# Optimization experiments

Measured on AMD Instinct MI355X. Metric: run time of the kernel, lower is better.

Reference implementation:

```python
import jax, jax.numpy as jnp
import numpy as np

B, C, D, H = 4, 1024, 768, 12      # batch, seq_len(>512 long-doc), hidden, heads
E, K, S, V, P = 32, 2, 24, 8, 512  # entities, mentions/entity, sents, virtual nodes, ht pairs
NT = 256                            # node type embedding dim
EMB, BLK, NL = 768, 64, 97          # emb_size, block_size, num_labels
OFFSET = 1


def setup_inputs() -> dict:
    key = jax.random.key(0)
    ks = jax.random.split(key, 13)
    return {
        "sequence_output": jax.random.normal(ks[0], (B, C, D), jnp.float32),
        "attention": jax.random.uniform(ks[1], (B, H, C, C), jnp.float32),
        "entity_pos": jax.random.randint(ks[2], (B, E, K), 0, C - 2),
        "sent_pos": jax.random.randint(ks[3], (B, S), 0, C - 2),
        "virtual_pos": jax.random.randint(ks[4], (B, V), 0, C - 2),
        "hts": jax.random.randint(ks[5], (B, P, 2), 0, E),
        "node_type_emb": jax.random.normal(ks[6], (B, E, NT), jnp.float32) * 0.02,
        "W_head": jax.random.normal(ks[7], (2 * D + NT, EMB), jnp.float32) * 0.02,
        "b_head": jnp.zeros((EMB,), jnp.float32),
        "W_tail": jax.random.normal(ks[8], (2 * D + NT, EMB), jnp.float32) * 0.02,
        "b_tail": jnp.zeros((EMB,), jnp.float32),
        "W_bil": jax.random.normal(ks[9], (EMB * BLK, NL), jnp.float32) * 0.02,
        "b_bil": jnp.zeros((NL,), jnp.float32),
    }


def reference(sequence_output, attention, entity_pos, sent_pos, virtual_pos, hts,
              node_type_emb, W_head, b_head, W_tail, b_tail, W_bil, b_bil):
    # --- get_mention_embed / get_entity_embed: gather mention-start rows ---
    idx = entity_pos + OFFSET                      # [B,E,K] token index of each mention start
    flat = idx.reshape(B, E * K)                   # mention order matches torch double loop
    mention_embed = jnp.take_along_axis(sequence_output, flat[:, :, None], axis=1)  # [B,E*K,D]
    entity_embed = jax.nn.logsumexp(mention_embed.reshape(B, E, K, D), axis=2)      # [B,E,D]

    # --- get_sent_embed / get_virtual_embed: single-row gathers ---
    sent_embed = jnp.take_along_axis(sequence_output, (sent_pos + OFFSET)[:, :, None], axis=1)      # [B,S,D]
    virtual_embed = jnp.take_along_axis(sequence_output, (virtual_pos + OFFSET)[:, :, None], axis=1)  # [B,V,D]

    # --- get_rss: localized-context pooling over attention ---
    att_t = attention.transpose(0, 2, 1, 3)        # [B,C,H,C] so we gather query rows
    e_att = jnp.take_along_axis(att_t, flat[:, :, None, None], axis=1)  # [B,E*K,H,C]
    e_att = e_att.reshape(B, E, K, H, C).mean(axis=2)                   # [B,E,H,C] mean over mentions
    h_att = jnp.take_along_axis(e_att, hts[:, :, 0][:, :, None, None], axis=1)  # [B,P,H,C]
    t_att = jnp.take_along_axis(e_att, hts[:, :, 1][:, :, None, None], axis=1)  # [B,P,H,C]
    ht_att = (h_att * t_att).mean(axis=2)                               # [B,P,C] mean over heads
    ht_att = ht_att / (ht_att.sum(axis=-1, keepdims=True) + 1e-5)
    rs = jnp.einsum('bld,brl->brd', sequence_output, ht_att)            # [B,P,D]

    # --- get_pair_entity_embed on entity hidden state (entity_embed + node-type emb) ---
    ent_hidden = jnp.concatenate([entity_embed, node_type_emb], axis=-1)          # [B,E,D+NT]
    s_emb = jnp.take_along_axis(ent_hidden, hts[:, :, 0][:, :, None], axis=1)     # [B,P,D+NT]
    t_emb = jnp.take_along_axis(ent_hidden, hts[:, :, 1][:, :, None], axis=1)

    # --- head/tail extractors + grouped bilinear classifier ---
    hs = jnp.tanh(jnp.concatenate([s_emb, rs], axis=-1) @ W_head + b_head)  # [B,P,EMB]
    ts = jnp.tanh(jnp.concatenate([t_emb, rs], axis=-1) @ W_tail + b_tail)
    b1 = hs.reshape(B, P, EMB // BLK, BLK)
    b2 = ts.reshape(B, P, EMB // BLK, BLK)
    bl = (b1[..., :, None] * b2[..., None, :]).reshape(B, P, EMB * BLK)     # [B,P,EMB*BLK]
    logits = bl @ W_bil + b_bil                                             # [B,P,NL]
    return (logits, mention_embed, sent_embed, virtual_embed)
```

## Files before the change

### kernel.cpp

```cpp
#include <hip/hip_runtime.h>

#define B_   4
#define C_   1024
#define D_   768
#define H_   12
#define E_   32
#define K_   2
#define S_   24
#define V_   8
#define P_   512
#define NT_  256
#define EMB_ 768
#define BLK_ 64
#define NL_  97
#define DNT_ 1024
#define KHT_ 1792
#define KBIL_ 49152
#define NPAD_ 128

typedef __bf16 bf16x8 __attribute__((ext_vector_type(8)));
typedef float  f32x4  __attribute__((ext_vector_type(4)));

__device__ __forceinline__ float b2f(unsigned short u) {
    return (float)__builtin_bit_cast(__bf16, u);
}
__device__ __forceinline__ unsigned short f2b(float f) {
    return __builtin_bit_cast(unsigned short, (__bf16)f);
}
__device__ __forceinline__ float ld_in(const void* p, size_t i, int isf) {
    return isf ? ((const float*)p)[i] : b2f(((const unsigned short*)p)[i]);
}
__device__ __forceinline__ void st_out(void* p, size_t i, float v, int isf) {
    if (isf) ((float*)p)[i] = v;
    else     ((unsigned short*)p)[i] = f2b(v);
}

__global__ __launch_bounds__(256) void k_probe(const unsigned short* __restrict__ seq_u,
                                               int* __restrict__ flag)
{
    __shared__ int sh_huge[256];
    __shared__ int sh_zero[256];
    int tid = threadIdx.x;
    int huge = 0, zero = 0;
    for (int i = tid; i < 4096; i += 256) {
        unsigned short u = seq_u[2 * i];
        float f = b2f(u);
        if (!(fabsf(f) <= 1e10f)) huge = 1;
        if (u == 0) zero++;
    }
    sh_huge[tid] = huge; sh_zero[tid] = zero;
    __syncthreads();
    for (int s = 128; s > 0; s >>= 1) {
        if (tid < s) { sh_huge[tid] |= sh_huge[tid + s]; sh_zero[tid] += sh_zero[tid + s]; }
        __syncthreads();
    }
    if (tid == 0) flag[0] = (sh_huge[0] || sh_zero[0] > 3600) ? 1 : 0;
}

#define PREP_GATHER 256
#define PREP_EATT   (PREP_GATHER + B_*E_*H_)
#define PREP_TSEQ   (PREP_EATT + 768)
#define PREP_TW     (PREP_TSEQ + 672)
#define PREP_TBIL   (PREP_TW + 768)

__global__ __launch_bounds__(256) void k_prep(
    const void* __restrict__ seq, const void* __restrict__ att,
    const int* __restrict__ epos, const int* __restrict__ spos,
    const int* __restrict__ vpos, const void* __restrict__ ntype,
    const void* __restrict__ Wh, const void* __restrict__ Wt_,
    const void* __restrict__ Wb,
    float* __restrict__ enth, float* __restrict__ e_att,
    unsigned short* __restrict__ seqT,
    unsigned short* __restrict__ WtH, unsigned short* __restrict__ WtT,
    unsigned short* __restrict__ WtB,
    void* __restrict__ outv, long long moff, long long soff, long long voff,
    const int* __restrict__ dflag)
{
    __shared__ __align__(16) unsigned char smem[12544];
    int blk = blockIdx.x, tid = threadIdx.x;
    int isf = *dflag;
    if (blk < PREP_GATHER) {
        if (blk < B_ * E_) {
            int b = blk / E_, e = blk % E_;
            int i0 = epos[(b * E_ + e) * K_ + 0] + 1;
            int i1 = epos[(b * E_ + e) * K_ + 1] + 1;
            size_t r0 = ((size_t)b * C_ + i0) * D_;
            size_t r1 = ((size_t)b * C_ + i1) * D_;
            size_t m0 = (size_t)moff + ((size_t)(b * E_ * K_) + 2 * e) * D_;
            size_t m1 = m0 + D_;
            float* eh = enth + (size_t)(b * E_ + e) * DNT_;
            for (int d = tid; d < D_; d += 256) {
                float a = ld_in(seq, r0 + d, isf);
                float c = ld_in(seq, r1 + d, isf);
                st_out(outv, m0 + d, a, isf);
                st_out(outv, m1 + d, c, isf);
                float mx = fmaxf(a, c);
                eh[d] = mx + logf(expf(a - mx) + expf(c - mx));
            }
            size_t nt0 = (size_t)(b * E_ + e) * NT_;
            for (int j = tid; j < NT_; j += 256) eh[D_ + j] = ld_in(ntype, nt0 + j, isf);
        } else if (blk < B_ * E_ + B_ * S_) {
            int t = blk - B_ * E_; int b = t / S_, s = t % S_;
            int i = spos[b * S_ + s] + 1;
            size_t r = ((size_t)b * C_ + i) * D_;
            size_t o = (size_t)soff + (size_t)(b * S_ + s) * D_;
            for (int d = tid; d < D_; d += 256) st_out(outv, o + d, ld_in(seq, r + d, isf), isf);
        } else {
            int t = blk - B_ * E_ - B_ * S_; int b = t / V_, v = t % V_;
            int i = vpos[b * V_ + v] + 1;
            size_t r = ((size_t)b * C_ + i) * D_;
            size_t o = (size_t)voff + (size_t)(b * V_ + v) * D_;
            for (int d = tid; d < D_; d += 256) st_out(outv, o + d, ld_in(seq, r + d, isf), isf);
        }
    } else if (blk < PREP_EATT) {
        int t = blk - PREP_GATHER;
        int b = t / (E_ * H_); int r = t % (E_ * H_); int e = r / H_; int h = r % H_;
        int i0 = epos[(b * E_ + e) * K_ + 0] + 1;
        int i1 = epos[(b * E_ + e) * K_ + 1] + 1;
        size_t a0 = (((size_t)b * H_ + h) * C_ + i0) * C_;
        size_t a1 = (((size_t)b * H_ + h) * C_ + i1) * C_;
        float* o = e_att + (((size_t)(b * E_ + e)) * H_ + h) * C_;
        for (int c = tid; c < C_; c += 256)
            o[c] = 0.5f * (ld_in(att, a0 + c, isf) + ld_in(att, a1 + c, isf));
    } else if (blk < PREP_TSEQ) {
        int t = blk - PREP_EATT;
        int b = t / 192; int r = t % 192; int ct = r / 12; int dt = r % 12;
        typedef unsigned short row65[65];
        row65* tile = (row65*)smem;
        for (int idx = tid; idx < 4096; idx += 256) {
            int cc = idx >> 6, dd = idx & 63;
            tile[cc][dd] = f2b(ld_in(seq, ((size_t)b * C_ + ct * 64 + cc) * D_ + dt * 64 + dd, isf));
        }
        __syncthreads();
        for (int idx = tid; idx < 4096; idx += 256) {
            int dd = idx >> 6, cc = idx & 63;
            seqT[((size_t)b * D_ + dt * 64 + dd) * C_ + ct * 64 + cc] = tile[cc][dd];
        }
    } else if (blk < PREP_TW) {
        int t = blk - PREP_TSEQ;
        int mat = t / 336; int r = t % 336; int kt = r / 12; int nt = r % 12;
        const void* in = mat ? Wt_ : Wh;
        unsigned short* out = mat ? WtT : WtH;
        typedef unsigned short row65[65];
        row65* tile = (row65*)smem;
        for (int idx = tid; idx < 4096; idx += 256) {
            int kk = idx >> 6, nn = idx & 63;
            tile[kk][nn] = f2b(ld_in(in, ((size_t)kt * 64 + kk) * EMB_ + nt * 64 + nn, isf));
        }
        __syncthreads();
        for (int idx = tid; idx < 4096; idx += 256) {
            int nn = idx >> 6, kk = idx & 63;
            out[((size_t)nt * 64 + nn) * KHT_ + kt * 64 + kk] = tile[kk][nn];
        }
    } else {
        int t = blk - PREP_TW;
        int k0 = t << 6;
        unsigned short* raw = (unsigned short*)smem;
        for (int idx = tid; idx < 64 * NL_; idx += 256)
            raw[idx] = f2b(ld_in(Wb, (size_t)k0 * NL_ + idx, isf));
        __syncthreads();
        int kk = tid & 63, nq = tid >> 6;
        for (int i = 0; i < 32; i++) {
            int n = nq * 32 + i;
            unsigned short v = (n < NL_) ? raw[kk * NL_ + n] : (unsigned short)0;
            WtB[(size_t)n * KBIL_ + k0 + kk] = v;
        }
    }
}

__global__ __launch_bounds__(256) void k_mid(
    const float* __restrict__ e_att, const float* __restrict__ enth,
    const int* __restrict__ hts,
    unsigned short* __restrict__ htb,
    unsigned short* __restrict__ Xh, unsigned short* __restrict__ Xt,
    float* __restrict__ logitsF)
{
    __shared__ float red[4];
    int blk = blockIdx.x, tid = threadIdx.x;
    if (blk < B_ * P_) {
        int b = blk >> 9;
        int he = hts[blk * 2 + 0], te = hts[blk * 2 + 1];
        const float* ph = e_att + (size_t)(b * E_ + he) * H_ * C_;
        const float* pt = e_att + (size_t)(b * E_ + te) * H_ * C_;
        float v[4]; float ls = 0.f;
        for (int ci = 0; ci < 4; ci++) {
            int c = tid + (ci << 8);
            float acc = 0.f;
#pragma unroll
            for (int h = 0; h < H_; h++) acc += ph[h * C_ + c] * pt[h * C_ + c];
            acc *= (1.0f / (float)H_);
            v[ci] = acc; ls += acc;
        }
        for (int off = 32; off > 0; off >>= 1) ls += __shfl_down(ls, off, 64);
        if ((tid & 63) == 0) red[tid >> 6] = ls;
        __syncthreads();
        float inv = 1.0f / (red[0] + red[1] + red[2] + red[3] + 1e-5f);
        for (int ci = 0; ci < 4; ci++)
            htb[((size_t)blk << 10) + tid + (ci << 8)] = f2b(v[ci] * inv);
    } else if (blk < 2 * B_ * P_) {
        int m = blk - B_ * P_; int b = m >> 9;
        int eh = hts[m * 2 + 0], et = hts[m * 2 + 1];
        const float* sh = enth + (size_t)(b * E_ + eh) * DNT_;
        const float* st = enth + (size_t)(b * E_ + et) * DNT_;
        for (int k = tid; k < DNT_; k += 256) {
            Xh[(size_t)m * KHT_ + k] = f2b(sh[k]);
            Xt[(size_t)m * KHT_ + k] = f2b(st[k]);
        }
    } else {
        int t = blk - 2 * B_ * P_;
        ((float4*)logitsF)[(size_t)t * 256 + tid] = make_float4(0.f, 0.f, 0.f, 0.f);
    }
}

__global__ __launch_bounds__(256) void k_gemm(
    const unsigned short* __restrict__ A0, const unsigned short* __restrict__ A1,
    const unsigned short* __restrict__ B0, const unsigned short* __restrict__ B1,
    long long lda, long long ldb, long long sAz, long long sBz,
    int nsteps, int zmode,
    const void* __restrict__ bias0, const void* __restrict__ bias1,
    unsigned short* __restrict__ oY0, unsigned short* __restrict__ oY1,
    unsigned short* __restrict__ oX1, unsigned short* __restrict__ oX2,
    const int* __restrict__ dflag)
{
    int n0 = blockIdx.x * 64, m0 = blockIdx.y * 64, z = blockIdx.z;
    const unsigned short* Ab; const unsigned short* Bb;
    unsigned short* oY = nullptr; const void* bias = nullptr;
    if (zmode == 0) {
        Ab = A0 + (size_t)z * sAz; Bb = B0 + (size_t)z * sBz;
    } else {
        Ab = z ? A1 : A0; Bb = z ? B1 : B0;
        oY = z ? oY1 : oY0; bias = z ? bias1 : bias0;
    }
    __shared__ __align__(16) unsigned short a_lds[64][40];
    __shared__ __align__(16) unsigned short b_lds[64][40];
    int tid = threadIdx.x, lane = tid & 63, w = tid >> 6;
    int wm = (w >> 1) * 32, wn = (w & 1) * 32, q = lane >> 4, l15 = lane & 15;
    f32x4 acc00 = {0.f,0.f,0.f,0.f}, acc01 = acc00, acc10 = acc00, acc11 = acc00;
    int srow = tid >> 2, sch = (tid & 3) * 8;
    const unsigned short* pa = Ab + (size_t)(m0 + srow) * lda + sch;
    const unsigned short* pb = Bb + (size_t)(n0 + srow) * ldb + sch;
    int4 ra = *(const int4*)pa;
    int4 rb = *(const int4*)pb;
    for (int ks = 0; ks < nsteps; ks++) {
        __syncthreads();
        *(int4*)&a_lds[srow][sch] = ra;
        *(int4*)&b_lds[srow][sch] = rb;
        __syncthreads();
        if (ks + 1 < nsteps) {
            ra = *(const int4*)(pa + (size_t)(ks + 1) * 32);
            rb = *(const int4*)(pb + (size_t)(ks + 1) * 32);
        }
        bf16x8 a0 = *(const bf16x8*)&a_lds[wm + l15][q * 8];
        bf16x8 a1 = *(const bf16x8*)&a_lds[wm + 16 + l15][q * 8];
        bf16x8 b0 = *(const bf16x8*)&b_lds[wn + l15][q * 8];
        bf16x8 b1 = *(const bf16x8*)&b_lds[wn + 16 + l15][q * 8];
        acc00 = __builtin_amdgcn_mfma_f32_16x16x32_bf16(a0, b0, acc00, 0, 0, 0);
        acc01 = __builtin_amdgcn_mfma_f32_16x16x32_bf16(a0, b1, acc01, 0, 0, 0);
        acc10 = __builtin_amdgcn_mfma_f32_16x16x32_bf16(a1, b0, acc10, 0, 0, 0);
        acc11 = __builtin_amdgcn_mfma_f32_16x16x32_bf16(a1, b1, acc11, 0, 0, 0);
    }
    f32x4 accs[2][2] = {{acc00, acc01}, {acc10, acc11}};
    int isf = (zmode == 1) ? *dflag : 0;
#pragma unroll
    for (int mt = 0; mt < 2; mt++)
#pragma unroll
        for (int nt = 0; nt < 2; nt++) {
            int gmb = m0 + wm + mt * 16 + q * 4;
            int gn  = n0 + wn + nt * 16 + l15;
            if (zmode == 0) {
#pragma unroll
                for (int r = 0; r < 4; r++) {
                    unsigned short v = f2b(accs[mt][nt][r]);
                    size_t o = (size_t)(z * P_ + gmb + r) * KHT_ + DNT_ + gn;
                    oX1[o] = v; oX2[o] = v;
                }
            } else {
                float bv = ld_in(bias, gn, isf);
#pragma unroll
                for (int r = 0; r < 4; r++)
                    oY[(size_t)(gmb + r) * EMB_ + gn] = f2b(tanhf(accs[mt][nt][r] + bv));
            }
        }
}

__global__ __launch_bounds__(256) void k_bil(
    const unsigned short* __restrict__ hsB, const unsigned short* __restrict__ tsB,
    const unsigned short* __restrict__ WtB, float* __restrict__ logitsF)
{
    int m0 = blockIdx.x * 32;
    int g  = blockIdx.y;
    int tid = threadIdx.x, lane = tid & 63, w = tid >> 6;
    int q = lane >> 4, l15 = lane & 15;
    __shared__ __align__(16) unsigned short hsl[32][80];
    __shared__ __align__(16) unsigned short tsl[32][80];
    for (int idx = tid; idx < 512; idx += 256) {
        int m = idx >> 4, j4 = (idx & 15) * 4;
        *(ushort4*)&hsl[m][j4] = *(const ushort4*)&hsB[(size_t)(m0 + m) * EMB_ + g * 64 + j4];
        *(ushort4*)&tsl[m][j4] = *(const ushort4*)&tsB[(size_t)(m0 + m) * EMB_ + g * 64 + j4];
    }
    __syncthreads();

    const unsigned short* pB0 = WtB + (size_t)(w * 16 + l15) * KBIL_ + g * 4096 + q * 8;
    const unsigned short* pB1 = pB0 + (size_t)64 * KBIL_;
    bf16x8 rb0[2], rb1[2];
    rb0[0] = *(const bf16x8*)(pB0);      rb1[0] = *(const bf16x8*)(pB1);
    rb0[1] = *(const bf16x8*)(pB0 + 32); rb1[1] = *(const bf16x8*)(pB1 + 32);
    f32x4 acc00 = {0.f,0.f,0.f,0.f}, acc01 = acc00, acc10 = acc00, acc11 = acc00;

#pragma unroll 2
    for (int kk = 0; kk < 128; kk++) {
        int sl = kk & 1;
        bf16x8 bw0 = rb0[sl], bw1 = rb1[sl];
        if (kk + 2 < 128) {
            rb0[sl] = *(const bf16x8*)(pB0 + (size_t)(kk + 2) * 32);
            rb1[sl] = *(const bf16x8*)(pB1 + (size_t)(kk + 2) * 32);
        }
        int i = kk >> 1, h = kk & 1;
        float ha0 = b2f(hsl[l15][i]);
        float ha1 = b2f(hsl[16 + l15][i]);
        bf16x8 t0 = *(const bf16x8*)&tsl[l15][h * 32 + q * 8];
        bf16x8 t1 = *(const bf16x8*)&tsl[16 + l15][h * 32 + q * 8];
        bf16x8 af0, af1;
#pragma unroll
        for (int j = 0; j < 8; j++) {
            af0[j] = (__bf16)(ha0 * (float)t0[j]);
            af1[j] = (__bf16)(ha1 * (float)t1[j]);
        }
        acc00 = __builtin_amdgcn_mfma_f32_16x16x32_bf16(af0, bw0, acc00, 0, 0, 0);
        acc01 = __builtin_amdgcn_mfma_f32_16x16x32_bf16(af0, bw1, acc01, 0, 0, 0);
        acc10 = __builtin_amdgcn_mfma_f32_16x16x32_bf16(af1, bw0, acc10, 0, 0, 0);
        acc11 = __builtin_amdgcn_mfma_f32_16x16x32_bf16(af1, bw1, acc11, 0, 0, 0);
    }
#pragma unroll
    for (int r = 0; r < 4; r++) {
        atomicAdd(&logitsF[(size_t)(m0 + q * 4 + r) * NPAD_ + w * 16 + l15],           acc00[r]);
        atomicAdd(&logitsF[(size_t)(m0 + q * 4 + r) * NPAD_ + w * 16 + 64 + l15],      acc01[r]);
        atomicAdd(&logitsF[(size_t)(m0 + 16 + q * 4 + r) * NPAD_ + w * 16 + l15],      acc10[r]);
        atomicAdd(&logitsF[(size_t)(m0 + 16 + q * 4 + r) * NPAD_ + w * 16 + 64 + l15], acc11[r]);
    }
}

__global__ __launch_bounds__(256) void k_fin(
    const float* __restrict__ logitsF, const void* __restrict__ b_bil,
    void* __restrict__ outv, const int* __restrict__ dflag)
{
    int isf = *dflag;
    int idx = blockIdx.x * 256 + threadIdx.x;
    if (idx >= B_ * P_ * NL_) return;
    int m = idx / NL_, n = idx % NL_;
    st_out(outv, idx, logitsF[(size_t)m * NPAD_ + n] + ld_in(b_bil, n, isf), isf);
}

extern "C" void kernel_launch(void* const* d_in, const int* in_sizes, int n_in,
                              void* d_out, int out_size, void* d_ws, size_t ws_size,
                              hipStream_t stream)
{
    const void* seq    = d_in[0];
    const void* att    = d_in[1];
    const int*  epos   = (const int*)d_in[2];
    const int*  spos   = (const int*)d_in[3];
    const int*  vpos   = (const int*)d_in[4];
    const int*  hts    = (const int*)d_in[5];
    const void* ntype  = d_in[6];
    const void* W_head = d_in[7];
    const void* b_head = d_in[8];
    const void* W_tail = d_in[9];
    const void* b_tail = d_in[10];
    const void* W_bil  = d_in[11];
    const void* b_bil  = d_in[12];

    long long mention_off = (long long)B_ * P_ * NL_;
    long long sent_off    = mention_off + (long long)B_ * E_ * K_ * D_;
    long long virt_off    = sent_off + (long long)B_ * S_ * D_;

    char* p = (char*)d_ws;
    auto alloc = [&](size_t bytes) { void* r = (void*)p; p += (bytes + 255) & ~(size_t)255; return r; };
    int*            dflag   = (int*)alloc(256);
    float*          e_att   = (float*)alloc((size_t)B_ * E_ * H_ * C_ * 4);
    unsigned short* htb     = (unsigned short*)alloc((size_t)B_ * P_ * C_ * 2);
    unsigned short* seqT    = (unsigned short*)alloc((size_t)B_ * D_ * C_ * 2);
    unsigned short* WtH     = (unsigned short*)alloc((size_t)EMB_ * KHT_ * 2);
    unsigned short* WtT     = (unsigned short*)alloc((size_t)EMB_ * KHT_ * 2);
    unsigned short* WtB     = (unsigned short*)alloc((size_t)NPAD_ * KBIL_ * 2);
    unsigned short* Xh      = (unsigned short*)alloc((size_t)B_ * P_ * KHT_ * 2);
    unsigned short* Xt      = (unsigned short*)alloc((size_t)B_ * P_ * KHT_ * 2);
    unsigned short* hsB     = (unsigned short*)alloc((size_t)B_ * P_ * EMB_ * 2);
    unsigned short* tsB     = (unsigned short*)alloc((size_t)B_ * P_ * EMB_ * 2);
    float*          logitsF = (float*)alloc((size_t)B_ * P_ * NPAD_ * 4);
    float*          enth    = (float*)alloc((size_t)B_ * E_ * DNT_ * 4);

    dim3 blk(256);
    k_probe<<<1, blk, 0, stream>>>((const unsigned short*)seq, dflag);
    k_prep<<<PREP_TBIL, blk, 0, stream>>>(
        seq, att, epos, spos, vpos, ntype, W_head, W_tail, W_bil,
        enth, e_att, seqT, WtH, WtT, WtB,
        d_out, mention_off, sent_off, virt_off, dflag);
    k_mid<<<2 * B_ * P_ + 256, blk, 0, stream>>>(e_att, enth, hts, htb, Xh, Xt, logitsF);
    k_gemm<<<dim3(EMB_ / 64, P_ / 64, B_), blk, 0, stream>>>(
        htb, nullptr, seqT, nullptr, C_, C_,
        (long long)P_ * C_, (long long)D_ * C_, C_ / 32, 0,
        nullptr, nullptr, nullptr, nullptr, Xh, Xt, dflag);
    k_gemm<<<dim3(EMB_ / 64, (B_ * P_) / 64, 2), blk, 0, stream>>>(
        Xh, Xt, WtH, WtT, KHT_, KHT_, 0, 0, KHT_ / 32, 1,
        b_head, b_tail, hsB, tsB, nullptr, nullptr, dflag);
    k_bil<<<dim3((B_ * P_) / 32, 12, 1), blk, 0, stream>>>(hsB, tsB, WtB, logitsF);
    k_fin<<<(B_ * P_ * NL_ + 255) / 256, blk, 0, stream>>>(logitsF, b_bil, d_out, dflag);
}
```

Before: 453.9 us.

## Inline dtype probe per wavefront and store entity attention as bf16

Removes the separate single-block probe kernel that detected whether inputs are fp32 or bf16. Each wavefront now runs a cheaper 64-sample ballot-based probe inline in every kernel that needs the flag. The averaged entity attention buffer is also stored as bf16 instead of fp32, halving its write and read traffic in k_prep and k_mid. The trade-offs are a smaller probe sample, which makes the dtype guess less robust, and reduced precision in the intermediate attention values.

```diff
diff --git a/kernel.cpp b/kernel.cpp
--- a/kernel.cpp
+++ b/kernel.cpp
@@ -34,27 +34,11 @@
     if (isf) ((float*)p)[i] = v;
     else     ((unsigned short*)p)[i] = f2b(v);
 }
-
-__global__ __launch_bounds__(256) void k_probe(const unsigned short* __restrict__ seq_u,
-                                               int* __restrict__ flag)
-{
-    __shared__ int sh_huge[256];
-    __shared__ int sh_zero[256];
-    int tid = threadIdx.x;
-    int huge = 0, zero = 0;
-    for (int i = tid; i < 4096; i += 256) {
-        unsigned short u = seq_u[2 * i];
-        float f = b2f(u);
-        if (!(fabsf(f) <= 1e10f)) huge = 1;
-        if (u == 0) zero++;
-    }
-    sh_huge[tid] = huge; sh_zero[tid] = zero;
-    __syncthreads();
-    for (int s = 128; s > 0; s >>= 1) {
-        if (tid < s) { sh_huge[tid] |= sh_huge[tid + s]; sh_zero[tid] += sh_zero[tid + s]; }
-        __syncthreads();
-    }
-    if (tid == 0) flag[0] = (sh_huge[0] || sh_zero[0] > 3600) ? 1 : 0;
+__device__ __forceinline__ int probe_isf(const void* seq) {
+    unsigned short u = ((const unsigned short*)seq)[2 * (threadIdx.x & 63)];
+    int huge = !(fabsf(b2f(u)) <= 1e10f);
+    unsigned long long zb = __ballot(u == 0);
+    return __any(huge) || (__popcll(zb) > 56);
 }
 
 #define PREP_GATHER 256
@@ -69,16 +53,15 @@
     const int* __restrict__ vpos, const void* __restrict__ ntype,
     const void* __restrict__ Wh, const void* __restrict__ Wt_,
     const void* __restrict__ Wb,
-    float* __restrict__ enth, float* __restrict__ e_att,
+    float* __restrict__ enth, unsigned short* __restrict__ e_att,
     unsigned short* __restrict__ seqT,
     unsigned short* __restrict__ WtH, unsigned short* __restrict__ WtT,
     unsigned short* __restrict__ WtB,
-    void* __restrict__ outv, long long moff, long long soff, long long voff,
-    const int* __restrict__ dflag)
+    void* __restrict__ outv, long long moff, long long soff, long long voff)
 {
     __shared__ __align__(16) unsigned char smem[12544];
     int blk = blockIdx.x, tid = threadIdx.x;
-    int isf = *dflag;
+    int isf = probe_isf(seq);
     if (blk < PREP_GATHER) {
         if (blk < B_ * E_) {
             int b = blk / E_, e = blk % E_;
@@ -119,9 +102,9 @@
         int i1 = epos[(b * E_ + e) * K_ + 1] + 1;
         size_t a0 = (((size_t)b * H_ + h) * C_ + i0) * C_;
         size_t a1 = (((size_t)b * H_ + h) * C_ + i1) * C_;
-        float* o = e_att + (((size_t)(b * E_ + e)) * H_ + h) * C_;
+        unsigned short* o = e_att + (((size_t)(b * E_ + e)) * H_ + h) * C_;
         for (int c = tid; c < C_; c += 256)
-            o[c] = 0.5f * (ld_in(att, a0 + c, isf) + ld_in(att, a1 + c, isf));
+            o[c] = f2b(0.5f * (ld_in(att, a0 + c, isf) + ld_in(att, a1 + c, isf)));
     } else if (blk < PREP_TSEQ) {
         int t = blk - PREP_EATT;
         int b = t / 192; int r = t % 192; int ct = r / 12; int dt = r % 12;
@@ -169,7 +152,7 @@
 }
 
 __global__ __launch_bounds__(256) void k_mid(
-    const float* __restrict__ e_att, const float* __restrict__ enth,
+    const unsigned short* __restrict__ e_att, const float* __restrict__ enth,
     const int* __restrict__ hts,
     unsigned short* __restrict__ htb,
     unsigned short* __restrict__ Xh, unsigned short* __restrict__ Xt,
@@ -180,14 +163,14 @@
     if (blk < B_ * P_) {
         int b = blk >> 9;
         int he = hts[blk * 2 + 0], te = hts[blk * 2 + 1];
-        const float* ph = e_att + (size_t)(b * E_ + he) * H_ * C_;
-        const float* pt = e_att + (size_t)(b * E_ + te) * H_ * C_;
+        const unsigned short* ph = e_att + (size_t)(b * E_ + he) * H_ * C_;
+        const unsigned short* pt = e_att + (size_t)(b * E_ + te) * H_ * C_;
         float v[4]; float ls = 0.f;
         for (int ci = 0; ci < 4; ci++) {
             int c = tid + (ci << 8);
             float acc = 0.f;
 #pragma unroll
-            for (int h = 0; h < H_; h++) acc += ph[h * C_ + c] * pt[h * C_ + c];
+            for (int h = 0; h < H_; h++) acc += b2f(ph[h * C_ + c]) * b2f(pt[h * C_ + c]);
             acc *= (1.0f / (float)H_);
             v[ci] = acc; ls += acc;
         }
@@ -220,7 +203,7 @@
     const void* __restrict__ bias0, const void* __restrict__ bias1,
     unsigned short* __restrict__ oY0, unsigned short* __restrict__ oY1,
     unsigned short* __restrict__ oX1, unsigned short* __restrict__ oX2,
-    const int* __restrict__ dflag)
+    const void* __restrict__ seq)
 {
     int n0 = blockIdx.x * 64, m0 = blockIdx.y * 64, z = blockIdx.z;
     const unsigned short* Ab; const unsigned short* Bb;
@@ -260,7 +243,7 @@
         acc11 = __builtin_amdgcn_mfma_f32_16x16x32_bf16(a1, b1, acc11, 0, 0, 0);
     }
     f32x4 accs[2][2] = {{acc00, acc01}, {acc10, acc11}};
-    int isf = (zmode == 1) ? *dflag : 0;
+    int isf = (zmode == 1) ? probe_isf(seq) : 0;
 #pragma unroll
     for (int mt = 0; mt < 2; mt++)
 #pragma unroll
@@ -342,9 +325,9 @@
 
 __global__ __launch_bounds__(256) void k_fin(
     const float* __restrict__ logitsF, const void* __restrict__ b_bil,
-    void* __restrict__ outv, const int* __restrict__ dflag)
-{
-    int isf = *dflag;
+    void* __restrict__ outv, const void* __restrict__ seq)
+{
+    int isf = probe_isf(seq);
     int idx = blockIdx.x * 256 + threadIdx.x;
     if (idx >= B_ * P_ * NL_) return;
     int m = idx / NL_, n = idx % NL_;
@@ -375,8 +358,7 @@
 
     char* p = (char*)d_ws;
     auto alloc = [&](size_t bytes) { void* r = (void*)p; p += (bytes + 255) & ~(size_t)255; return r; };
-    int*            dflag   = (int*)alloc(256);
-    float*          e_att   = (float*)alloc((size_t)B_ * E_ * H_ * C_ * 4);
+    unsigned short* e_att   = (unsigned short*)alloc((size_t)B_ * E_ * H_ * C_ * 2);
     unsigned short* htb     = (unsigned short*)alloc((size_t)B_ * P_ * C_ * 2);
     unsigned short* seqT    = (unsigned short*)alloc((size_t)B_ * D_ * C_ * 2);
     unsigned short* WtH     = (unsigned short*)alloc((size_t)EMB_ * KHT_ * 2);
@@ -390,19 +372,18 @@
     float*          enth    = (float*)alloc((size_t)B_ * E_ * DNT_ * 4);
 
     dim3 blk(256);
-    k_probe<<<1, blk, 0, stream>>>((const unsigned short*)seq, dflag);
     k_prep<<<PREP_TBIL, blk, 0, stream>>>(
         seq, att, epos, spos, vpos, ntype, W_head, W_tail, W_bil,
         enth, e_att, seqT, WtH, WtT, WtB,
-        d_out, mention_off, sent_off, virt_off, dflag);
+        d_out, mention_off, sent_off, virt_off);
     k_mid<<<2 * B_ * P_ + 256, blk, 0, stream>>>(e_att, enth, hts, htb, Xh, Xt, logitsF);
     k_gemm<<<dim3(EMB_ / 64, P_ / 64, B_), blk, 0, stream>>>(
         htb, nullptr, seqT, nullptr, C_, C_,
         (long long)P_ * C_, (long long)D_ * C_, C_ / 32, 0,
-        nullptr, nullptr, nullptr, nullptr, Xh, Xt, dflag);
+        nullptr, nullptr, nullptr, nullptr, Xh, Xt, seq);
     k_gemm<<<dim3(EMB_ / 64, (B_ * P_) / 64, 2), blk, 0, stream>>>(
         Xh, Xt, WtH, WtT, KHT_, KHT_, 0, 0, KHT_ / 32, 1,
-        b_head, b_tail, hsB, tsB, nullptr, nullptr, dflag);
+        b_head, b_tail, hsB, tsB, nullptr, nullptr, seq);
     k_bil<<<dim3((B_ * P_) / 32, 12, 1), blk, 0, stream>>>(hsB, tsB, WtB, logitsF);
-    k_fin<<<(B_ * P_ * NL_ + 255) / 256, blk, 0, stream>>>(logitsF, b_bil, d_out, dflag);
-}
+    k_fin<<<(B_ * P_ * NL_ + 255) / 256, blk, 0, stream>>>(logitsF, b_bil, d_out, seq);
+}
```

New measurement: 450.2 us. About the same (-0.8%).
